# Kernel optimization log

Measured on AMD Instinct MI355X. Metric: run time of the kernel, lower is better.

## Reference

```python
import jax, jax.numpy as jnp
import numpy as np

B, N, E, D, OUT, L = 4, 10000, 160000, 128, 64, 4
NEG = 0.01  # LeakyReLU slope

def lrelu(x):
    return jnp.where(x > 0, x, NEG * x)

def setup_inputs() -> dict:
    key = jax.random.key(0)
    ks = jax.random.split(key, 20)
    s = 0.05
    inp = {
        "x": jax.random.normal(ks[0], (B, N * 3), dtype=jnp.float32),
        "edge_index": jax.random.randint(ks[1], (2, E), 0, N, dtype=jnp.int32),
        # f0: Linear(3, D)
        "w0": jax.random.normal(ks[2], (3, D), dtype=jnp.float32) * s,
        "b0": jax.random.normal(ks[3], (D,), dtype=jnp.float32) * s,
        # per-layer params stacked on leading L axis
        "ew1": jax.random.normal(ks[4], (L, 2 * D + 1, D), dtype=jnp.float32) * s,
        "eb1": jax.random.normal(ks[5], (L, D), dtype=jnp.float32) * s,
        "ew2": jax.random.normal(ks[6], (L, D, D), dtype=jnp.float32) * s,
        "eb2": jax.random.normal(ks[7], (L, D), dtype=jnp.float32) * s,
        "cw": jax.random.normal(ks[8], (L, D, 1), dtype=jnp.float32) * s,
        "cb": jax.random.normal(ks[9], (L, 1), dtype=jnp.float32) * s,
        "nw1": jax.random.normal(ks[10], (L, 2 * D, D), dtype=jnp.float32) * s,
        "nb1": jax.random.normal(ks[11], (L, D), dtype=jnp.float32) * s,
        "nw2": jax.random.normal(ks[12], (L, D, D), dtype=jnp.float32) * s,
        "nb2": jax.random.normal(ks[13], (L, D), dtype=jnp.float32) * s,
        # project: Linear(D, OUT)
        "wp": jax.random.normal(ks[14], (D, OUT), dtype=jnp.float32) * s,
        "bp": jax.random.normal(ks[15], (OUT,), dtype=jnp.float32) * s,
    }
    return inp

def reference(x, edge_index, w0, b0, ew1, eb1, ew2, eb2, cw, cb, nw1, nb1, nw2, nb2, wp, bp):
    b = x.shape[0]
    n = x.shape[1] // 3
    pos = x.reshape(b, n, 3)            # coordinates [B,N,3]
    h = lrelu(pos @ w0 + b0)            # node features [B,N,D]
    row, col = edge_index[0], edge_index[1]
    # per-node in-edge counts (same for all layers/batches); scatter_mean -> 0 for empty nodes
    cnt = jnp.zeros((n,), x.dtype).at[col].add(1.0)
    denom = jnp.maximum(cnt, 1.0)[None, :, None]
    for i in range(L):
        rel = pos[:, row] - pos[:, col]                          # [B,E,3]
        dist_sq = jnp.sum(rel * rel, axis=-1, keepdims=True)     # [B,E,1]
        edge_in = jnp.concatenate([h[:, row], h[:, col], dist_sq], axis=-1)  # [B,E,2D+1]
        msg = lrelu(lrelu(edge_in @ ew1[i] + eb1[i]) @ ew2[i] + eb2[i])       # [B,E,D]
        aggr = jnp.zeros((b, n, msg.shape[-1]), msg.dtype).at[:, col].add(msg) / denom  # scatter_mean
        coord_update = jnp.tanh(aggr @ cw[i] + cb[i])            # [B,N,1]
        pos = pos + coord_update * 0.1
        node_in = jnp.concatenate([h, aggr], axis=-1)            # [B,N,2D]
        h = h + lrelu(lrelu(node_in @ nw1[i] + nb1[i]) @ nw2[i] + nb2[i])
    return lrelu(h.mean(axis=1) @ wp + bp)                       # [B,OUT]
```

## Files before the change

### kernel.cpp

```cpp
#include <hip/hip_runtime.h>
#include <hip/hip_bf16.h>
#include <math.h>

#define BB   4
#define NN   10000
#define NP   10112
#define EE   160000
#define DD   128
#define OUTD 64
#define LL   4
#define NEGS 0.01f
#define MSTR 136
#define RSF  34

typedef __attribute__((ext_vector_type(8))) short   short8;
typedef __attribute__((ext_vector_type(4))) float   floatx4;
typedef __attribute__((ext_vector_type(4))) uint    uintx4;

__device__ __forceinline__ float lrelu(float x) { return fmaxf(x, NEGS * x); }
__device__ __forceinline__ ushort f2bf(float x) {
    uint u = __builtin_bit_cast(uint, x);
    return (ushort)((u + 0x7FFFu + ((u >> 16) & 1u)) >> 16);
}
__device__ __forceinline__ float bf2f(ushort u) {
    uint v = ((uint)u) << 16;
    return __builtin_bit_cast(float, v);
}
__device__ __forceinline__ float bcf(uint u) { return __builtin_bit_cast(float, u); }

__global__ void k_cvtw_all(const float* __restrict__ ew1, const float* __restrict__ ew2,
                           const float* __restrict__ nw1, const float* __restrict__ nw2,
                           ushort* __restrict__ wtopf, ushort* __restrict__ wmidf,
                           ushort* __restrict__ ew2f, ushort* __restrict__ nw1f,
                           ushort* __restrict__ nw2f) {
    int tid = blockIdx.x * 256 + threadIdx.x;
    const float* src; ushort* dst; int pitch, nks, loc;
    if (tid < 8192)       { src = ew1;                     dst = wtopf; pitch = 257; nks = 4; loc = tid; }
    else if (tid < 16384) { src = ew1 + (size_t)128 * DD;  dst = wmidf; pitch = 257; nks = 4; loc = tid - 8192; }
    else if (tid < 24576) { src = ew2;                     dst = ew2f;  pitch = 128; nks = 4; loc = tid - 16384; }
    else if (tid < 40960) { src = nw1;                     dst = nw1f;  pitch = 256; nks = 8; loc = tid - 24576; }
    else                  { src = nw2;                     dst = nw2f;  pitch = 128; nks = 4; loc = tid - 40960; }
    int lane = loc & 63;
    int nt   = (loc >> 6) & 7;
    int ks   = (loc >> 9) % nks;
    int l    = loc / (nks * 512);
    int quad = lane >> 4, l16 = lane & 15;
    int n = nt * 16 + l16;
    const float* s = src + (size_t)l * pitch * DD;
    ushort* d = dst + (size_t)loc * 8;
    #pragma unroll
    for (int j = 0; j < 8; ++j)
        d[j] = f2bf(s[(size_t)(ks * 32 + quad * 8 + j) * DD + n]);
}

__global__ void k_h0(const float* __restrict__ x, const float* __restrict__ w0,
                     const float* __restrict__ b0, ushort* __restrict__ hb) {
    int idx = blockIdx.x * 256 + threadIdx.x;
    if (idx >= BB * NP * DD) return;
    int d  = idx & (DD - 1);
    int bn = idx >> 7;
    int n  = bn % NP, b = bn / NP;
    float v = 0.0f;
    if (n < NN) {
        const float* p = x + ((size_t)b * NN + n) * 3;
        v = lrelu(b0[d] + p[0] * w0[d] + p[1] * w0[DD + d] + p[2] * w0[2 * DD + d]);
    }
    hb[idx] = f2bf(v);
}

__global__ void k_count(const int* __restrict__ col, float* __restrict__ cnt,
                        int* __restrict__ ecnt) {
    int e = blockIdx.x * blockDim.x + threadIdx.x;
    if (e < EE) {
        int c = col[e];
        atomicAdd(&cnt[c], 1.0f);
        atomicAdd(&ecnt[c], 1);
    }
}

__global__ __launch_bounds__(256) void k_scan(const int* __restrict__ ecnt,
                                              int* __restrict__ cursor) {
    __shared__ int s_sum[256];
    int t = threadIdx.x;
    int base = t * 40;
    int s = 0;
    for (int i = 0; i < 40; ++i) {
        int n = base + i;
        if (n < NN) s += ecnt[n];
    }
    s_sum[t] = s;
    __syncthreads();
    if (t == 0) {
        int a = 0;
        for (int i = 0; i < 256; ++i) { int v = s_sum[i]; s_sum[i] = a; a += v; }
    }
    __syncthreads();
    int a = s_sum[t];
    for (int i = 0; i < 40; ++i) {
        int n = base + i;
        if (n < NN) { cursor[n] = a; a += ecnt[n]; }
    }
}

__global__ void k_place(const int* __restrict__ row, const int* __restrict__ col,
                        int* __restrict__ cursor,
                        int* __restrict__ rowS, int* __restrict__ colS) {
    int e = blockIdx.x * blockDim.x + threadIdx.x;
    if (e >= EE) return;
    int c = col[e];
    int p = atomicAdd(&cursor[c], 1);
    rowS[p] = row[e];
    colS[p] = c;
}

__global__ __launch_bounds__(256) void k_pq(
    const ushort* __restrict__ hb, const ushort* __restrict__ wtf,
    const ushort* __restrict__ wmf, const float* __restrict__ b1,
    ushort* __restrict__ P, ushort* __restrict__ Q)
{
    __shared__ __align__(16) ushort s_out[64 * MSTR];
    const int g = blockIdx.x;
    const int b = (g & 7) >> 1;
    const int n0 = ((g >> 3) * 2 + (g & 1)) * 64;
    const int t = threadIdx.x;
    const int w = t >> 6, lane = t & 63, quad = lane >> 4, l16 = lane & 15;
    const int rw = w * 16;
    const int nw = n0 + rw;

    const ushort* hptr = hb + ((size_t)b * NP + nw + l16) * DD;
    float b1r[8];
    #pragma unroll
    for (int nt = 0; nt < 8; ++nt) b1r[nt] = b1[nt * 16 + l16];

    const short8* wt = (const short8*)wtf;
    const short8* wm = (const short8*)wmf;

    #pragma unroll
    for (int pass = 0; pass < 2; ++pass) {
        floatx4 ap[8];
        #pragma unroll
        for (int nt = 0; nt < 8; ++nt)
            #pragma unroll
            for (int r = 0; r < 4; ++r) ap[nt][r] = pass ? b1r[nt] : 0.0f;
        const short8* wv = pass ? wm : wt;
        #pragma unroll
        for (int ks = 0; ks < 4; ++ks) {
            short8 bf[8];
            #pragma unroll
            for (int nt = 0; nt < 8; ++nt) bf[nt] = wv[(ks * 8 + nt) * 64 + lane];
            short8 af = *(const short8*)(hptr + ks * 32 + quad * 8);
            #pragma unroll
            for (int nt = 0; nt < 8; ++nt)
                ap[nt] = __builtin_amdgcn_mfma_f32_16x16x32_bf16(af, bf[nt], ap[nt], 0, 0, 0);
        }
        #pragma unroll
        for (int nt = 0; nt < 8; ++nt)
            #pragma unroll
            for (int r = 0; r < 4; ++r)
                s_out[(rw + quad * 4 + r) * MSTR + nt * 16 + l16] = f2bf(ap[nt][r]);
        ushort* dst = pass ? Q : P;
        #pragma unroll
        for (int i = 0; i < 4; ++i) {
            int row = rw + i * 4 + quad;
            short8 v = *(const short8*)&s_out[row * MSTR + l16 * 8];
            *(short8*)(dst + ((size_t)b * NP + n0 + row) * DD + l16 * 8) = v;
        }
    }
}

__global__ __launch_bounds__(256, 4) void k_edge(
    const float* __restrict__ pos,
    const ushort* __restrict__ P, const ushort* __restrict__ Q,
    const int* __restrict__ rowS, const int* __restrict__ colS,
    const float* __restrict__ w1last,
    const ushort* __restrict__ w2f, const float* __restrict__ b2,
    float* __restrict__ aggr)
{
    __shared__ __align__(16) int    s_col[128];
    __shared__ __align__(16) float  s_ds[128];
    __shared__ __align__(16) float  s_red[128 * RSF];

    const int g    = blockIdx.x;
    const int b    = (g & 7) >> 1;
    const int tile = (g >> 3) * 2 + (g & 1);
    const int e0   = tile * 128;
    const int t    = threadIdx.x;
    const int w    = t >> 6, lane = t & 63;
    const int quad = lane >> 4, l16 = lane & 15;
    const int ew   = w * 32;

    const ushort* pp[2];
    const ushort* qp[2];
    #pragma unroll
    for (int mt = 0; mt < 2; ++mt) {
        int el = e0 + ew + mt * 16 + l16;
        pp[mt] = P + ((size_t)b * NP + rowS[el]) * DD;
        qp[mt] = Q + ((size_t)b * NP + colS[el]) * DD;
    }

    uintx4 pf[2][4], qf[2][4];
    #pragma unroll
    for (int ks = 0; ks < 4; ++ks) {
        const int koff = ks * 32 + quad * 8;
        #pragma unroll
        for (int mt = 0; mt < 2; ++mt) {
            pf[mt][ks] = *(const uintx4*)(pp[mt] + koff);
            qf[mt][ks] = *(const uintx4*)(qp[mt] + koff);
        }
    }

    if (t < 128) {
        int e = e0 + t;
        int r = rowS[e], c = colS[e];
        s_col[t] = c;
        const float* pr = pos + ((size_t)b * NN + r) * 3;
        const float* pc = pos + ((size_t)b * NN + c) * 3;
        float dx = pr[0] - pc[0], dy = pr[1] - pc[1], dz = pr[2] - pc[2];
        s_ds[t] = dx * dx + dy * dy + dz * dz;
    }
    __syncthreads();

    const int rh    = lane >> 5;
    const int colL  = lane & 31;
    const int rbase = ew + rh * 16;
    int bmask = 0, cid0;
    {
        int prev = s_col[rbase];
        cid0 = prev;
        #pragma unroll
        for (int r2 = 1; r2 < 16; ++r2) {
            int c = s_col[rbase + r2];
            if (c != prev) bmask |= (1 << r2);
            prev = c;
        }
    }

    float dsv[2];
    #pragma unroll
    for (int mt = 0; mt < 2; ++mt) dsv[mt] = s_ds[ew + mt * 16 + l16];

    uintx4 mid[2][4];
    #pragma unroll
    for (int ks = 0; ks < 4; ++ks) {
        const int koff = ks * 32 + quad * 8;
        floatx4 wl0 = *(const floatx4*)(w1last + koff);
        floatx4 wl1 = *(const floatx4*)(w1last + koff + 4);
        float wl[8] = {wl0[0], wl0[1], wl0[2], wl0[3], wl1[0], wl1[1], wl1[2], wl1[3]};
        #pragma unroll
        for (int mt = 0; mt < 2; ++mt) {
            #pragma unroll
            for (int i = 0; i < 4; ++i) {
                uint pv = pf[mt][ks][i], qv = qf[mt][ks][i];
                float vlo = lrelu(bcf(pv << 16) + bcf(qv << 16) + dsv[mt] * wl[2 * i]);
                float vhi = lrelu(bcf(pv & 0xFFFF0000u) + bcf(qv & 0xFFFF0000u) + dsv[mt] * wl[2 * i + 1]);
                mid[mt][ks][i] = __builtin_amdgcn_perm(
                    __builtin_bit_cast(uint, vhi), __builtin_bit_cast(uint, vlo), 0x07060302u);
            }
        }
    }

    float* aggr_bd = aggr + (size_t)b * NP * DD;

    const short8* w2v = (const short8*)w2f;
    #pragma unroll
    for (int ph = 0; ph < 2; ++ph) {
        float b2r4[4];
        #pragma unroll
        for (int ntl = 0; ntl < 4; ++ntl) b2r4[ntl] = b2[(ph * 4 + ntl) * 16 + l16];

        floatx4 acc[2][4];
        #pragma unroll
        for (int mt = 0; mt < 2; ++mt)
            #pragma unroll
            for (int ntl = 0; ntl < 4; ++ntl)
                #pragma unroll
                for (int r = 0; r < 4; ++r) acc[mt][ntl][r] = b2r4[ntl];

        #pragma unroll
        for (int ks = 0; ks < 4; ++ks) {
            short8 bf[4];
            #pragma unroll
            for (int ntl = 0; ntl < 4; ++ntl)
                bf[ntl] = w2v[(ks * 8 + ph * 4 + ntl) * 64 + lane];
            #pragma unroll
            for (int mt = 0; mt < 2; ++mt) {
                short8 af = __builtin_bit_cast(short8, mid[mt][ks]);
                #pragma unroll
                for (int ntl = 0; ntl < 4; ++ntl)
                    acc[mt][ntl] = __builtin_amdgcn_mfma_f32_16x16x32_bf16(af, bf[ntl], acc[mt][ntl], 0, 0, 0);
            }
        }

        #pragma unroll
        for (int sp = 0; sp < 2; ++sp) {
            #pragma unroll
            for (int mt = 0; mt < 2; ++mt)
                #pragma unroll
                for (int j = 0; j < 2; ++j) {
                    const int ntl = sp * 2 + j;
                    #pragma unroll
                    for (int r = 0; r < 4; ++r)
                        s_red[(ew + mt * 16 + quad * 4 + r) * RSF + j * 16 + l16] =
                            lrelu(acc[mt][ntl][r]);
                }

            const int d = ph * 64 + sp * 32 + colL;
            float* ab = aggr_bd + d;
            float run = 0.0f;
            int cid = cid0;
            #pragma unroll
            for (int r = 0; r < 16; ++r) {
                float v = s_red[(rbase + r) * RSF + colL];
                if (bmask & (1 << r)) {
                    atomicAdd(ab + (size_t)cid * DD, run);
                    run = 0.0f;
                    cid = s_col[rbase + r];
                }
                run += v;
            }
            atomicAdd(ab + (size_t)cid * DD, run);
        }
    }
}

__global__ __launch_bounds__(256) void k_node(
    ushort* hb, float* aggr, const float* __restrict__ cnt,
    const float* __restrict__ cw, const float* __restrict__ cb,
    const ushort* __restrict__ w1f, const float* __restrict__ b1,
    const ushort* __restrict__ w2f, const float* __restrict__ b2,
    float* __restrict__ pos,
    int do_pq,
    const ushort* __restrict__ wtn, const ushort* __restrict__ wmn,
    const float* __restrict__ b1n,
    ushort* __restrict__ P, ushort* __restrict__ Q)
{
    __shared__ __align__(16) ushort s_mid[64 * MSTR];
    __shared__ __align__(16) ushort s_ho[64 * MSTR];

    const int g    = blockIdx.x;
    const int b    = (g & 7) >> 1;
    const int n0   = ((g >> 3) * 2 + (g & 1)) * 64;
    const int t    = threadIdx.x;
    const int w    = t >> 6, lane = t & 63;
    const int quad = lane >> 4, l16 = lane & 15;
    const int rw   = w * 16;
    const int nw   = n0 + rw;
    const int w2i  = w * 2;

    #pragma unroll
    for (int i = 0; i < 4; ++i) {
        int row = rw + i * 4 + quad;
        short8 v = *(const short8*)(hb + ((size_t)b * NP + n0 + row) * DD + l16 * 8);
        *(short8*)&s_ho[row * MSTR + l16 * 8] = v;
    }

    float* aptr = aggr + ((size_t)b * NP + nw + l16) * DD;
    float inv = 0.0f;
    {
        int node = nw + l16;
        if (node < NN) { float dn = cnt[node]; inv = 1.0f / fmaxf(dn, 1.0f); }
    }
    float b1r[8];
    #pragma unroll
    for (int nt = 0; nt < 8; ++nt) b1r[nt] = b1[nt * 16 + l16];
    float b2r2[2];
    #pragma unroll
    for (int nt = 0; nt < 2; ++nt) b2r2[nt] = b2[(w2i + nt) * 16 + l16];

    floatx4 acc[8];
    #pragma unroll
    for (int nt = 0; nt < 8; ++nt)
        #pragma unroll
        for (int r = 0; r < 4; ++r) acc[nt][r] = b1r[nt];

    float cwacc = 0.0f;
    const floatx4 zero4 = {0.0f, 0.0f, 0.0f, 0.0f};
    const short8* w1v = (const short8*)w1f;
    #pragma unroll
    for (int ks = 0; ks < 8; ++ks) {
        short8 bf[8];
        #pragma unroll
        for (int nt = 0; nt < 8; ++nt) bf[nt] = w1v[(ks * 8 + nt) * 64 + lane];
        const int koff = (ks & 3) * 32 + quad * 8;
        if (ks < 4) {
            short8 af = *(const short8*)(&s_ho[(rw + l16) * MSTR + koff]);
            #pragma unroll
            for (int nt = 0; nt < 8; ++nt)
                acc[nt] = __builtin_amdgcn_mfma_f32_16x16x32_bf16(af, bf[nt], acc[nt], 0, 0, 0);
        } else {
            floatx4 cw0 = *(const floatx4*)(cw + koff);
            floatx4 cw1 = *(const floatx4*)(cw + koff + 4);
            floatx4 a0 = *(const floatx4*)(aptr + koff);
            floatx4 a1 = *(const floatx4*)(aptr + koff + 4);
            *(floatx4*)(aptr + koff)     = zero4;
            *(floatx4*)(aptr + koff + 4) = zero4;
            short8 af;
            #pragma unroll
            for (int j = 0; j < 4; ++j) {
                float v = a0[j] * inv;
                af[j] = (short)f2bf(v);
                cwacc += v * cw0[j];
            }
            #pragma unroll
            for (int j = 0; j < 4; ++j) {
                float v = a1[j] * inv;
                af[4 + j] = (short)f2bf(v);
                cwacc += v * cw1[j];
            }
            #pragma unroll
            for (int nt = 0; nt < 8; ++nt)
                acc[nt] = __builtin_amdgcn_mfma_f32_16x16x32_bf16(af, bf[nt], acc[nt], 0, 0, 0);
        }
    }

    {
        float full = cwacc;
        full += __shfl_xor(full, 16);
        full += __shfl_xor(full, 32);
        int node = nw + l16;
        if (quad == 0 && node < NN) {
            float cu = 0.1f * tanhf(full + cb[0]);
            float* pp = pos + ((size_t)b * NN + node) * 3;
            pp[0] += cu; pp[1] += cu; pp[2] += cu;
        }
    }

    #pragma unroll
    for (int nt = 0; nt < 8; ++nt)
        #pragma unroll
        for (int r = 0; r < 4; ++r)
            s_mid[(rw + quad * 4 + r) * MSTR + nt * 16 + l16] = f2bf(lrelu(acc[nt][r]));

    __syncthreads();

    floatx4 acc2[4][2];
    #pragma unroll
    for (int rt = 0; rt < 4; ++rt)
        #pragma unroll
        for (int nt = 0; nt < 2; ++nt)
            #pragma unroll
            for (int r = 0; r < 4; ++r) acc2[rt][nt][r] = b2r2[nt];

    const short8* w2v = (const short8*)w2f;
    #pragma unroll
    for (int ks = 0; ks < 4; ++ks) {
        short8 bfc[2];
        #pragma unroll
        for (int nt = 0; nt < 2; ++nt)
            bfc[nt] = w2v[(ks * 8 + w2i + nt) * 64 + lane];
        #pragma unroll
        for (int rt = 0; rt < 4; ++rt) {
            short8 af = *(const short8*)(&s_mid[(rt * 16 + l16) * MSTR + ks * 32 + quad * 8]);
            #pragma unroll
            for (int nt = 0; nt < 2; ++nt)
                acc2[rt][nt] = __builtin_amdgcn_mfma_f32_16x16x32_bf16(af, bfc[nt], acc2[rt][nt], 0, 0, 0);
        }
    }

    __syncthreads();

    #pragma unroll
    for (int rt = 0; rt < 4; ++rt)
        #pragma unroll
        for (int nt = 0; nt < 2; ++nt)
            #pragma unroll
            for (int r = 0; r < 4; ++r) {
                int row = rt * 16 + quad * 4 + r;
                int col = w2i * 16 + nt * 16 + l16;
                float hold = bf2f(s_ho[row * MSTR + col]);
                s_mid[row * MSTR + col] = f2bf(hold + lrelu(acc2[rt][nt][r]));
            }

    __syncthreads();

    #pragma unroll
    for (int i = 0; i < 4; ++i) {
        int row = rw + i * 4 + quad;
        int n = n0 + row;
        short8 v = *(const short8*)&s_mid[row * MSTR + l16 * 8];
        if (n < NN)
            *(short8*)(hb + ((size_t)b * NP + n) * DD + l16 * 8) = v;
    }

    if (do_pq) {
        const short8* wt = (const short8*)wtn;
        const short8* wm = (const short8*)wmn;
        float b1nr2[2];
        #pragma unroll
        for (int nt = 0; nt < 2; ++nt) b1nr2[nt] = b1n[(w2i + nt) * 16 + l16];

        #pragma unroll
        for (int pass = 0; pass < 2; ++pass) {
            floatx4 ap[4][2];
            #pragma unroll
            for (int rt = 0; rt < 4; ++rt)
                #pragma unroll
                for (int nt = 0; nt < 2; ++nt)
                    #pragma unroll
                    for (int r = 0; r < 4; ++r) ap[rt][nt][r] = pass ? b1nr2[nt] : 0.0f;
            const short8* wv = pass ? wm : wt;
            #pragma unroll
            for (int ks = 0; ks < 4; ++ks) {
                short8 bfp[2];
                #pragma unroll
                for (int nt = 0; nt < 2; ++nt)
                    bfp[nt] = wv[(ks * 8 + w2i + nt) * 64 + lane];
                #pragma unroll
                for (int rt = 0; rt < 4; ++rt) {
                    short8 af = *(const short8*)(&s_mid[(rt * 16 + l16) * MSTR + ks * 32 + quad * 8]);
                    #pragma unroll
                    for (int nt = 0; nt < 2; ++nt)
                        ap[rt][nt] = __builtin_amdgcn_mfma_f32_16x16x32_bf16(af, bfp[nt], ap[rt][nt], 0, 0, 0);
                }
            }
            if (pass) __syncthreads();
            #pragma unroll
            for (int rt = 0; rt < 4; ++rt)
                #pragma unroll
                for (int nt = 0; nt < 2; ++nt)
                    #pragma unroll
                    for (int r = 0; r < 4; ++r)
                        s_ho[(rt * 16 + quad * 4 + r) * MSTR + w2i * 16 + nt * 16 + l16] =
                            f2bf(ap[rt][nt][r]);
            __syncthreads();
            ushort* dst = pass ? Q : P;
            #pragma unroll
            for (int i = 0; i < 4; ++i) {
                int row = rw + i * 4 + quad;
                short8 v = *(const short8*)&s_ho[row * MSTR + l16 * 8];
                *(short8*)(dst + ((size_t)b * NP + n0 + row) * DD + l16 * 8) = v;
            }
        }
    }
}

#define NPC 50
__global__ void k_mean(const ushort* __restrict__ hb, float* __restrict__ hm) {
    int b  = blockIdx.y;
    int n0 = blockIdx.x * NPC;
    int d  = threadIdx.x;
    float s = 0.0f;
    for (int n = n0; n < n0 + NPC; ++n) s += bf2f(hb[((size_t)b * NP + n) * DD + d]);
    atomicAdd(&hm[b * DD + d], s);
}

__global__ void k_proj(const float* __restrict__ hm, const float* __restrict__ wp,
                       const float* __restrict__ bp, float* __restrict__ out) {
    int t = threadIdx.x;
    int b = t >> 6, o = t & (OUTD - 1);
    float s = 0.0f;
    for (int d2 = 0; d2 < DD; ++d2) s += hm[b * DD + d2] * wp[d2 * OUTD + o];
    s = s * (1.0f / NN) + bp[o];
    out[b * OUTD + o] = lrelu(s);
}

extern "C" void kernel_launch(void* const* d_in, const int* in_sizes, int n_in,
                              void* d_out, int out_size, void* d_ws, size_t ws_size,
                              hipStream_t stream) {
    (void)in_sizes; (void)n_in; (void)out_size; (void)ws_size;
    const float* x   = (const float*)d_in[0];
    const int*   ei  = (const int*)d_in[1];
    const float* w0  = (const float*)d_in[2];
    const float* b0  = (const float*)d_in[3];
    const float* ew1 = (const float*)d_in[4];
    const float* eb1 = (const float*)d_in[5];
    const float* ew2 = (const float*)d_in[6];
    const float* eb2 = (const float*)d_in[7];
    const float* cw  = (const float*)d_in[8];
    const float* cb  = (const float*)d_in[9];
    const float* nw1 = (const float*)d_in[10];
    const float* nb1 = (const float*)d_in[11];
    const float* nw2 = (const float*)d_in[12];
    const float* nb2 = (const float*)d_in[13];
    const float* wp  = (const float*)d_in[14];
    const float* bp  = (const float*)d_in[15];
    const int* row = ei;
    const int* col = ei + EE;

    const size_t HSZ = (size_t)BB * NP * DD;
    float* ws   = (float*)d_ws;
    float* aggr = ws;
    float* pos  = aggr + HSZ;
    float* cnt  = pos + (size_t)BB * NN * 3;
    float* hm   = cnt + NN;
    ushort* hb    = (ushort*)(hm + 512);
    ushort* Pb    = hb + HSZ;
    ushort* Qb    = Pb + HSZ;
    ushort* wtopf = Qb + HSZ;
    ushort* wmidf = wtopf + (size_t)LL * 16384;
    ushort* ew2f  = wmidf + (size_t)LL * 16384;
    ushort* nw1f  = ew2f + (size_t)LL * 16384;
    ushort* nw2f  = nw1f + (size_t)LL * 32768;
    int* ecnt   = (int*)(nw2f + (size_t)LL * 16384);
    int* cursor = ecnt + NN;
    int* rowS   = cursor + NN;
    int* colS   = rowS + EE;

    hipMemcpyAsync(pos, x, sizeof(float) * (size_t)BB * NN * 3,
                   hipMemcpyDeviceToDevice, stream);
    hipMemsetAsync(cnt, 0, sizeof(float) * NN, stream);
    hipMemsetAsync(ecnt, 0, sizeof(int) * NN, stream);
    hipMemsetAsync(hm, 0, sizeof(float) * BB * DD, stream);
    hipMemsetAsync(aggr, 0, sizeof(float) * HSZ, stream);

    k_cvtw_all<<<192, 256, 0, stream>>>(ew1, ew2, nw1, nw2,
                                        wtopf, wmidf, ew2f, nw1f, nw2f);

    k_h0<<<((int)HSZ + 255) / 256, 256, 0, stream>>>(x, w0, b0, hb);
    k_count<<<(EE + 255) / 256, 256, 0, stream>>>(col, cnt, ecnt);
    k_scan<<<1, 256, 0, stream>>>(ecnt, cursor);
    k_place<<<(EE + 255) / 256, 256, 0, stream>>>(row, col, cursor, rowS, colS);

    k_pq<<<(NP / 64) * BB, 256, 0, stream>>>(hb, wtopf, wmidf, eb1, Pb, Qb);

    for (int i = 0; i < LL; ++i) {
        k_edge<<<(EE / 128) * BB, 256, 0, stream>>>(
            pos, Pb, Qb, rowS, colS,
            ew1 + (size_t)i * 257 * DD + (size_t)256 * DD,
            ew2f + (size_t)i * 16384,
            eb2 + (size_t)i * DD,
            aggr);
        int nx = (i < LL - 1) ? (i + 1) : i;
        k_node<<<(NP / 64) * BB, 256, 0, stream>>>(
            hb, aggr, cnt,
            cw + (size_t)i * DD, cb + i,
            nw1f + (size_t)i * 32768, nb1 + (size_t)i * DD,
            nw2f + (size_t)i * 16384, nb2 + (size_t)i * DD,
            pos,
            (i < LL - 1) ? 1 : 0,
            wtopf + (size_t)nx * 16384, wmidf + (size_t)nx * 16384,
            eb1 + (size_t)nx * DD,
            Pb, Qb);
    }

    k_mean<<<dim3(NN / NPC, BB), DD, 0, stream>>>(hb, hm);
    k_proj<<<1, 256, 0, stream>>>(hm, wp, bp, (float*)d_out);
}
```

Before: 574.3 us.

## Split edge kernel into gather kernel and GEMM-scatter kernel via workspace buffer

```diff
diff --git a/kernel.cpp b/kernel.cpp
--- a/kernel.cpp
+++ b/kernel.cpp
@@ -168,7 +168,161 @@
     }
 }
 
-__global__ __launch_bounds__(256, 4) void k_edge(
+
+__global__ __launch_bounds__(256) void k_gath(
+    const float* __restrict__ pos,
+    const ushort* __restrict__ P, const ushort* __restrict__ Q,
+    const int* __restrict__ rowS, const int* __restrict__ colS,
+    const float* __restrict__ w1last,
+    ushort* __restrict__ mid)
+{
+    const int g    = blockIdx.x;
+    const int b    = g & 3;
+    const int e    = (g >> 2) * 32 + (threadIdx.x >> 3);
+    const int part = threadIdx.x & 7;
+    const int d0   = part * 16;
+
+    const int row = rowS[e], col = colS[e];
+    const float* pr = pos + ((size_t)b * NN + row) * 3;
+    const float* pc = pos + ((size_t)b * NN + col) * 3;
+    float dx = pr[0] - pc[0], dy = pr[1] - pc[1], dz = pr[2] - pc[2];
+    float ds = dx * dx + dy * dy + dz * dz;
+
+    const ushort* pp = P + ((size_t)b * NP + row) * DD + d0;
+    const ushort* qp = Q + ((size_t)b * NP + col) * DD + d0;
+    uintx4 pf0 = *(const uintx4*)(pp);
+    uintx4 pf1 = *(const uintx4*)(pp + 8);
+    uintx4 qf0 = *(const uintx4*)(qp);
+    uintx4 qf1 = *(const uintx4*)(qp + 8);
+
+    uintx4 out[2];
+    #pragma unroll
+    for (int h = 0; h < 2; ++h) {
+        uintx4 pv4 = h ? pf1 : pf0;
+        uintx4 qv4 = h ? qf1 : qf0;
+        floatx4 wl0 = *(const floatx4*)(w1last + d0 + h * 8);
+        floatx4 wl1 = *(const floatx4*)(w1last + d0 + h * 8 + 4);
+        float wl[8] = {wl0[0], wl0[1], wl0[2], wl0[3], wl1[0], wl1[1], wl1[2], wl1[3]};
+        #pragma unroll
+        for (int i = 0; i < 4; ++i) {
+            uint pv = pv4[i], qv = qv4[i];
+            float vlo = lrelu(bcf(pv << 16) + bcf(qv << 16) + ds * wl[2 * i]);
+            float vhi = lrelu(bcf(pv & 0xFFFF0000u) + bcf(qv & 0xFFFF0000u) + ds * wl[2 * i + 1]);
+            out[h][i] = __builtin_amdgcn_perm(
+                __builtin_bit_cast(uint, vhi), __builtin_bit_cast(uint, vlo), 0x07060302u);
+        }
+    }
+    ushort* mp = mid + ((size_t)b * EE + e) * DD + d0;
+    *(uintx4*)(mp)     = out[0];
+    *(uintx4*)(mp + 8) = out[1];
+}
+
+__global__ __launch_bounds__(256, 4) void k_gemm(
+    const int* __restrict__ colS,
+    const ushort* __restrict__ mid,
+    const ushort* __restrict__ w2f, const float* __restrict__ b2,
+    float* __restrict__ aggr)
+{
+    __shared__ __align__(16) int    s_col[128];
+    __shared__ __align__(16) float  s_red[128 * RSF];
+
+    const int g    = blockIdx.x;
+    const int b    = (g & 7) >> 1;
+    const int tile = (g >> 3) * 2 + (g & 1);
+    const int e0   = tile * 128;
+    const int t    = threadIdx.x;
+    const int w    = t >> 6, lane = t & 63;
+    const int quad = lane >> 4, l16 = lane & 15;
+    const int ew   = w * 32;
+
+    if (t < 128) s_col[t] = colS[e0 + t];
+    __syncthreads();
+
+    const int rh    = lane >> 5;
+    const int colL  = lane & 31;
+    const int rbase = ew + rh * 16;
+    int bmask = 0, cid0;
+    {
+        int prev = s_col[rbase];
+        cid0 = prev;
+        #pragma unroll
+        for (int r2 = 1; r2 < 16; ++r2) {
+            int c = s_col[rbase + r2];
+            if (c != prev) bmask |= (1 << r2);
+            prev = c;
+        }
+    }
+
+    const ushort* mrow[2];
+    #pragma unroll
+    for (int mt = 0; mt < 2; ++mt)
+        mrow[mt] = mid + ((size_t)b * EE + e0 + ew + mt * 16 + l16) * DD + quad * 8;
+
+    float* aggr_bd = aggr + (size_t)b * NP * DD;
+    const short8* w2v = (const short8*)w2f;
+
+    #pragma unroll
+    for (int ph = 0; ph < 2; ++ph) {
+        float b2r4[4];
+        #pragma unroll
+        for (int ntl = 0; ntl < 4; ++ntl) b2r4[ntl] = b2[(ph * 4 + ntl) * 16 + l16];
+
+        floatx4 acc[2][4];
+        #pragma unroll
+        for (int mt = 0; mt < 2; ++mt)
+            #pragma unroll
+            for (int ntl = 0; ntl < 4; ++ntl)
+                #pragma unroll
+                for (int r = 0; r < 4; ++r) acc[mt][ntl][r] = b2r4[ntl];
+
+        #pragma unroll
+        for (int ks = 0; ks < 4; ++ks) {
+            short8 bf[4];
+            #pragma unroll
+            for (int ntl = 0; ntl < 4; ++ntl)
+                bf[ntl] = w2v[(ks * 8 + ph * 4 + ntl) * 64 + lane];
+            #pragma unroll
+            for (int mt = 0; mt < 2; ++mt) {
+                short8 af = *(const short8*)(mrow[mt] + ks * 32);
+                #pragma unroll
+                for (int ntl = 0; ntl < 4; ++ntl)
+                    acc[mt][ntl] = __builtin_amdgcn_mfma_f32_16x16x32_bf16(af, bf[ntl], acc[mt][ntl], 0, 0, 0);
+            }
+        }
+
+        #pragma unroll
+        for (int sp = 0; sp < 2; ++sp) {
+            #pragma unroll
+            for (int mt = 0; mt < 2; ++mt)
+                #pragma unroll
+                for (int j = 0; j < 2; ++j) {
+                    const int ntl = sp * 2 + j;
+                    #pragma unroll
+                    for (int r = 0; r < 4; ++r)
+                        s_red[(ew + mt * 16 + quad * 4 + r) * RSF + j * 16 + l16] =
+                            lrelu(acc[mt][ntl][r]);
+                }
+
+            const int d = ph * 64 + sp * 32 + colL;
+            float* ab = aggr_bd + d;
+            float run = 0.0f;
+            int cid = cid0;
+            #pragma unroll
+            for (int r = 0; r < 16; ++r) {
+                float v = s_red[(rbase + r) * RSF + colL];
+                if (bmask & (1 << r)) {
+                    atomicAdd(ab + (size_t)cid * DD, run);
+                    run = 0.0f;
+                    cid = s_col[rbase + r];
+                }
+                run += v;
+            }
+            atomicAdd(ab + (size_t)cid * DD, run);
+        }
+    }
+}
+
+__global__ __launch_bounds__(256, 4) void k_edge_fused(
     const float* __restrict__ pos,
     const ushort* __restrict__ P, const ushort* __restrict__ Q,
     const int* __restrict__ rowS, const int* __restrict__ colS,
@@ -260,7 +414,6 @@
     }
 
     float* aggr_bd = aggr + (size_t)b * NP * DD;
-
     const short8* w2v = (const short8*)w2f;
     #pragma unroll
     for (int ph = 0; ph < 2; ++ph) {
@@ -557,7 +710,7 @@
 extern "C" void kernel_launch(void* const* d_in, const int* in_sizes, int n_in,
                               void* d_out, int out_size, void* d_ws, size_t ws_size,
                               hipStream_t stream) {
-    (void)in_sizes; (void)n_in; (void)out_size; (void)ws_size;
+    (void)in_sizes; (void)n_in; (void)out_size;
     const float* x   = (const float*)d_in[0];
     const int*   ei  = (const int*)d_in[1];
     const float* w0  = (const float*)d_in[2];
@@ -595,6 +748,10 @@
     int* cursor = ecnt + NN;
     int* rowS   = cursor + NN;
     int* colS   = rowS + EE;
+    ushort* midb = (ushort*)(colS + EE);
+
+    const size_t need = (size_t)((char*)(midb + (size_t)BB * EE * DD) - (char*)d_ws);
+    const bool use_split = (ws_size >= need);
 
     hipMemcpyAsync(pos, x, sizeof(float) * (size_t)BB * NN * 3,
                    hipMemcpyDeviceToDevice, stream);
@@ -614,12 +771,17 @@
     k_pq<<<(NP / 64) * BB, 256, 0, stream>>>(hb, wtopf, wmidf, eb1, Pb, Qb);
 
     for (int i = 0; i < LL; ++i) {
-        k_edge<<<(EE / 128) * BB, 256, 0, stream>>>(
-            pos, Pb, Qb, rowS, colS,
-            ew1 + (size_t)i * 257 * DD + (size_t)256 * DD,
-            ew2f + (size_t)i * 16384,
-            eb2 + (size_t)i * DD,
-            aggr);
+        const float* w1l = ew1 + (size_t)i * 257 * DD + (size_t)256 * DD;
+        if (use_split) {
+            k_gath<<<(EE / 32) * BB, 256, 0, stream>>>(
+                pos, Pb, Qb, rowS, colS, w1l, midb);
+            k_gemm<<<(EE / 128) * BB, 256, 0, stream>>>(
+                colS, midb, ew2f + (size_t)i * 16384, eb2 + (size_t)i * DD, aggr);
+        } else {
+            k_edge_fused<<<(EE / 128) * BB, 256, 0, stream>>>(
+                pos, Pb, Qb, rowS, colS, w1l,
+                ew2f + (size_t)i * 16384, eb2 + (size_t)i * DD, aggr);
+        }
         int nx = (i < LL - 1) ? (i + 1) : i;
         k_node<<<(NP / 64) * BB, 256, 0, stream>>>(
             hb, aggr, cnt,
```

After: 761.1 us. 1.33x slower.
